# Kernel tuning notes

Hardware: AMD Instinct MI355X
Metric: run time of the kernel (lower is better)

## Reference

```python
import jax, jax.numpy as jnp
import numpy as np

H = 16      # num_heads
D = 64      # head_dim
BQ = 64     # block_size_q
BKV = 64    # block_size_kv


def setup_inputs() -> dict:
    key = jax.random.key(0)
    ks = jax.random.split(key, 5)
    B, S, dim = 2, 2048, 1024
    x = jax.random.normal(ks[0], (B, S, dim), dtype=jnp.float32)
    Wq = jax.random.normal(ks[1], (dim, H * D), dtype=jnp.float32) * 0.02
    Wk = jax.random.normal(ks[2], (dim, H * D), dtype=jnp.float32) * 0.02
    Wv = jax.random.normal(ks[3], (dim, H * D), dtype=jnp.float32) * 0.02
    Wo = jax.random.normal(ks[4], (H * D, dim), dtype=jnp.float32) * 0.02
    return {"x": x, "Wq": Wq, "Wk": Wk, "Wv": Wv, "Wo": Wo}


def _flash_tiled(q, k, v, scale):
    # q,k,v: (B, H, S, D). Non-causal tiled attention with online softmax,
    # faithfully replicating the source's per-iteration division by l_new.
    B, nh, S, d = q.shape
    nq, nkv = S // BQ, S // BKV
    qb = q.reshape(B, nh, nq, BQ, d)                       # all q blocks at once (outer loop vectorized)
    kb = k.reshape(B, nh, nkv, BKV, d).transpose(2, 0, 1, 3, 4)  # (nkv, B, H, BKV, D)
    vb = v.reshape(B, nh, nkv, BKV, d).transpose(2, 0, 1, 3, 4)

    o0 = jnp.zeros((B, nh, nq, BQ, d), q.dtype)
    m0 = jnp.full((B, nh, nq, BQ), -jnp.inf, q.dtype)
    l0 = jnp.zeros((B, nh, nq, BQ), q.dtype)

    def step(carry, kv):
        o, m, l = carry
        kj, vj = kv
        s = jnp.einsum('bhnqd,bhkd->bhnqk', qb, kj) * scale   # (B,H,nq,BQ,BKV)
        m_new = jnp.maximum(m, s.max(axis=-1))
        p = jnp.exp(s - m_new[..., None])
        alpha = jnp.exp(m - m_new)
        l_new = alpha * l + p.sum(axis=-1)
        # NOTE: division by l_new every iteration, as in the source module.
        o_new = (alpha[..., None] * o + jnp.einsum('bhnqk,bhkd->bhnqd', p, vj)) / l_new[..., None]
        return (o_new, m_new, l_new), None

    (o, _, _), _ = jax.lax.scan(step, (o0, m0, l0), (kb, vb))
    return o.reshape(B, nh, S, d)


def reference(x, Wq, Wk, Wv, Wo):
    B, S, dim = x.shape
    scale = D ** -0.5
    q = (x @ Wq).reshape(B, S, H, D).transpose(0, 2, 1, 3)
    k = (x @ Wk).reshape(B, S, H, D).transpose(0, 2, 1, 3)
    v = (x @ Wv).reshape(B, S, H, D).transpose(0, 2, 1, 3)
    o = _flash_tiled(q, k, v, scale)                       # (B,H,S,D)
    out = o.transpose(0, 2, 1, 3).reshape(B, S, H * D)
    return out @ Wo
```

## Files before the change

### kernel.cpp

```cpp
#include <hip/hip_runtime.h>
#include <hip/hip_bf16.h>
#include <math.h>

#define BB   2
#define SS   2048
#define DIM  1024
#define NH   16
#define HD   64
#define MTOT (BB * SS)

typedef unsigned short ushortT;
typedef __attribute__((ext_vector_type(8))) short short8v;
typedef __attribute__((ext_vector_type(4))) float float4v;
typedef __attribute__((ext_vector_type(16))) float float16v;

union FragU { short8v v; unsigned short us[8]; unsigned int u[4]; };

__device__ inline unsigned short f2bf(float x) {
    unsigned u = __builtin_bit_cast(unsigned, x);
    u += 0x7fffu + ((u >> 16) & 1u);
    return (unsigned short)(u >> 16);
}
__device__ inline float bf2f(unsigned short h) {
    unsigned u = ((unsigned)h) << 16;
    return __builtin_bit_cast(float, u);
}
__device__ inline void split_tr(float x, unsigned short& hi, unsigned short& lo) {
    unsigned u = __builtin_bit_cast(unsigned, x);
    hi = (unsigned short)(u >> 16);
    float hf = __builtin_bit_cast(float, u & 0xffff0000u);
    lo = (unsigned short)(__builtin_bit_cast(unsigned, x - hf) >> 16);
}
__device__ inline void split4(const float4& x, short4& hi, short4& lo) {
    unsigned short h0 = f2bf(x.x), h1 = f2bf(x.y), h2 = f2bf(x.z), h3 = f2bf(x.w);
    hi = make_short4((short)h0, (short)h1, (short)h2, (short)h3);
    lo = make_short4((short)f2bf(x.x - bf2f(h0)), (short)f2bf(x.y - bf2f(h1)),
                     (short)f2bf(x.z - bf2f(h2)), (short)f2bf(x.w - bf2f(h3)));
}
__device__ inline void gld_lds16(const void* g, void* l) {
    __builtin_amdgcn_global_load_lds(
        (const __attribute__((address_space(1))) void*)g,
        (__attribute__((address_space(3))) void*)l, 16, 0, 0);
}
__device__ inline unsigned cvt_pk_bf16(float a, float b) {
    unsigned r;
    asm("v_cvt_pk_bf16_f32 %0, %1, %2" : "=v"(r) : "v"(a), "v"(b));
    return r;
}
__device__ inline void permlane32_swap(unsigned &a, unsigned &b) {
    asm("v_permlane32_swap_b32 %0, %1" : "+v"(a), "+v"(b));
}

__global__ __launch_bounds__(256) void convert_split_kernel(
    const float* __restrict__ in, ushortT* __restrict__ hi, ushortT* __restrict__ lo, int n4)
{
    int t = blockIdx.x * 256 + threadIdx.x;
    if (t < n4) {
        float4 x = ((const float4*)in)[t];
        short4 h, l; split4(x, h, l);
        ((short4*)hi)[t] = h;
        ((short4*)lo)[t] = l;
    }
}

__global__ __launch_bounds__(256) void transpose_split_kernel(
    const float* __restrict__ W0, const float* __restrict__ W1,
    const float* __restrict__ W2, const float* __restrict__ W3,
    ushortT* __restrict__ WtH, ushortT* __restrict__ WtL)
{
    const int z = blockIdx.z;
    const float* __restrict__ W = (z == 0) ? W0 : (z == 1) ? W1 : (z == 2) ? W2 : W3;
    ushortT* H = WtH + (size_t)z * 1024 * 1024;
    ushortT* L = WtL + (size_t)z * 1024 * 1024;

    __shared__ float T[64][65];
    const int k0 = blockIdx.y * 64, n0 = blockIdx.x * 64;
    const int tid = threadIdx.x;
    const int c4 = (tid & 15) * 4;

#pragma unroll
    for (int i = 0; i < 4; i++) {
        int r = (tid >> 4) + 16 * i;
        *(float4*)&T[r][c4] = *(const float4*)(W + (size_t)(k0 + r) * 1024 + n0 + c4);
    }
    __syncthreads();
#pragma unroll
    for (int i = 0; i < 4; i++) {
        int n = (tid >> 4) + 16 * i;
        float4 vv = make_float4(T[c4 + 0][n], T[c4 + 1][n], T[c4 + 2][n], T[c4 + 3][n]);
        short4 h, l; split4(vv, h, l);
        *(short4*)&H[(size_t)(n0 + n) * 1024 + k0 + c4] = h;
        *(short4*)&L[(size_t)(n0 + n) * 1024 + k0 + c4] = l;
    }
}

__global__ __launch_bounds__(256) void kv_convert_kernel(
    const float* __restrict__ kw,
    ushortT* __restrict__ KhG, ushortT* __restrict__ KlG)
{
    const int jb = blockIdx.x, bh = blockIdx.y;
    const int b = bh >> 4, h = bh & 15;

    __shared__ float T[64][68];
    const int tid = threadIdx.x;
    const size_t ibase = (size_t)b * SS * DIM + (size_t)h * HD + (size_t)(jb * 64) * DIM;
    const int c4 = (tid & 15) * 4;
#pragma unroll
    for (int i = 0; i < 4; i++) {
        int r = (tid >> 4) + 16 * i;
        *(float4*)&T[r][c4] = *(const float4*)(kw + ibase + (size_t)r * DIM + c4);
    }
    __syncthreads();

    ushortT* oh = KhG + (size_t)(bh * 32 + jb) * 4096;
    ushortT* ol = KlG + (size_t)(bh * 32 + jb) * 4096;

#pragma unroll
    for (int i = 0; i < 2; i++) {
        const int s = tid + i * 256;
        const int f = s >> 6;
        const int lane = s & 63;
        const int ds = f >> 1, kvt = f & 1;
        const int kv = kvt * 32 + (lane & 31);
        const int d0 = ds * 16 + (lane >> 5) * 8;
        ushortT hv[8], lv[8];
#pragma unroll
        for (int j = 0; j < 8; j++) split_tr(T[kv][d0 + j], hv[j], lv[j]);
        *(short4*)&oh[s * 8]     = *(short4*)&hv[0];
        *(short4*)&oh[s * 8 + 4] = *(short4*)&hv[4];
        *(short4*)&ol[s * 8]     = *(short4*)&lv[0];
        *(short4*)&ol[s * 8 + 4] = *(short4*)&lv[4];
    }
}

__global__ __launch_bounds__(256, 2) void gemm_bt_split_kernel(
    const ushortT* __restrict__ Ah, const ushortT* __restrict__ Al,
    const ushortT* __restrict__ BtH, const ushortT* __restrict__ BtL,
    float* __restrict__ Y0, float* __restrict__ Y1,
    ushortT* __restrict__ VhG, ushortT* __restrict__ VlG)
{
    const int z = blockIdx.z;
    const ushortT* __restrict__ Bh = BtH + (size_t)z * 1024 * 1024;
    const ushortT* __restrict__ Bl = BtL + (size_t)z * 1024 * 1024;

    const int K = 1024, N = 1024;
    const int m0 = blockIdx.y * 128;
    const int n0 = blockIdx.x * 128;

    __shared__ __align__(16) ushortT AhS[128 * 32];
    __shared__ __align__(16) ushortT AlS[128 * 32];
    __shared__ __align__(16) ushortT BhS[128 * 32];
    __shared__ __align__(16) ushortT BlS[128 * 32];

    const int tid  = threadIdx.x;
    const int wave = tid >> 6, lane = tid & 63;
    const int quad = lane >> 4, l15 = lane & 15;
    const int wm = wave >> 1, wn = wave & 1;

    const int s0 = tid, s1 = tid + 256;
    const int ar0 = s0 >> 2, ak0 = (s0 & 3) * 8;
    const int ar1 = s1 >> 2, ak1 = (s1 & 3) * 8;

    float4v acc[4][4];
#pragma unroll
    for (int i = 0; i < 4; i++)
#pragma unroll
        for (int j = 0; j < 4; j++) acc[i][j] = (float4v){0.f, 0.f, 0.f, 0.f};

    for (int k0 = 0; k0 < K; k0 += 32) {
        __syncthreads();
        gld_lds16(Ah + (size_t)(m0 + ar0) * K + k0 + ak0, &AhS[s0 * 8]);
        gld_lds16(Ah + (size_t)(m0 + ar1) * K + k0 + ak1, &AhS[s1 * 8]);
        gld_lds16(Al + (size_t)(m0 + ar0) * K + k0 + ak0, &AlS[s0 * 8]);
        gld_lds16(Al + (size_t)(m0 + ar1) * K + k0 + ak1, &AlS[s1 * 8]);
        gld_lds16(Bh + (size_t)(n0 + ar0) * K + k0 + ak0, &BhS[s0 * 8]);
        gld_lds16(Bh + (size_t)(n0 + ar1) * K + k0 + ak1, &BhS[s1 * 8]);
        gld_lds16(Bl + (size_t)(n0 + ar0) * K + k0 + ak0, &BlS[s0 * 8]);
        gld_lds16(Bl + (size_t)(n0 + ar1) * K + k0 + ak1, &BlS[s1 * 8]);
        __syncthreads();

        FragU ah[4], al[4], bh[4], bl[4];
#pragma unroll
        for (int t = 0; t < 4; t++) {
            ah[t].v = *(const short8v*)&AhS[(wm * 64 + t * 16 + l15) * 32 + quad * 8];
            al[t].v = *(const short8v*)&AlS[(wm * 64 + t * 16 + l15) * 32 + quad * 8];
            bh[t].v = *(const short8v*)&BhS[(wn * 64 + t * 16 + l15) * 32 + quad * 8];
            bl[t].v = *(const short8v*)&BlS[(wn * 64 + t * 16 + l15) * 32 + quad * 8];
        }
#pragma unroll
        for (int mt = 0; mt < 4; mt++)
#pragma unroll
            for (int nt = 0; nt < 4; nt++) {
                acc[mt][nt] = __builtin_amdgcn_mfma_f32_16x16x32_bf16(ah[mt].v, bh[nt].v, acc[mt][nt], 0, 0, 0);
                acc[mt][nt] = __builtin_amdgcn_mfma_f32_16x16x32_bf16(ah[mt].v, bl[nt].v, acc[mt][nt], 0, 0, 0);
                acc[mt][nt] = __builtin_amdgcn_mfma_f32_16x16x32_bf16(al[mt].v, bh[nt].v, acc[mt][nt], 0, 0, 0);
            }
    }

    if (z == 2) {
        const int b  = m0 >> 11;
        const int jb = ((m0 & 2047) >> 6) + wm;
        const int h  = (n0 >> 6) + wn;
        const size_t tb = (size_t)((b * 16 + h) * 32 + jb) * 4096;
        ushortT* vh = VhG + tb;
        ushortT* vl = VlG + tb;
#pragma unroll
        for (int mt = 0; mt < 4; mt++)
#pragma unroll
            for (int nt = 0; nt < 4; nt++) {
                const int off = ((((nt >> 1) * 4 + mt) * 64 +
                                  (quad >> 1) * 32 + (nt & 1) * 16 + l15) * 8) +
                                (quad & 1) * 4;
                float4 vv = make_float4(acc[mt][nt][0], acc[mt][nt][1],
                                        acc[mt][nt][2], acc[mt][nt][3]);
                unsigned short h0, l0, h1, l1, h2, l2, h3, l3;
                split_tr(vv.x, h0, l0); split_tr(vv.y, h1, l1);
                split_tr(vv.z, h2, l2); split_tr(vv.w, h3, l3);
                *(short4*)&vh[off] = make_short4((short)h0, (short)h1, (short)h2, (short)h3);
                *(short4*)&vl[off] = make_short4((short)l0, (short)l1, (short)l2, (short)l3);
            }
    } else {
        float* __restrict__ Y = (z == 0) ? Y0 : Y1;
#pragma unroll
        for (int mt = 0; mt < 4; mt++)
#pragma unroll
            for (int r = 0; r < 4; r++) {
                const int row = m0 + wm * 64 + mt * 16 + quad * 4 + r;
                float* yp = Y + (size_t)row * N + n0 + wn * 64 + l15;
#pragma unroll
                for (int nt = 0; nt < 4; nt++)
                    yp[nt * 16] = acc[mt][nt][r];
            }
    }
}

__global__ __launch_bounds__(256, 3) void attn_mfma_kernel(
    const float* __restrict__ q,
    const ushortT* __restrict__ KhG, const ushortT* __restrict__ KlG,
    const ushortT* __restrict__ VhG, const ushortT* __restrict__ VlG,
    ushortT* __restrict__ Oh, ushortT* __restrict__ Ol)
{
    __shared__ __align__(16) ushortT SMEM[16384];
    ushortT* KhS = SMEM;
    ushortT* KlS = SMEM + 4096;
    ushortT* VhS = SMEM + 8192;
    ushortT* VlS = SMEM + 12288;

    const int tid  = threadIdx.x;
    const int wave = tid >> 6, lane = tid & 63;
    const int l31 = lane & 31, hi5 = lane >> 5;
    const int bh = blockIdx.y, b = bh >> 4, h = bh & 15;
    const size_t base = (size_t)b * SS * DIM + (size_t)h * HD;
    const int qs0 = blockIdx.x * 128 + wave * 32;
    const int lane8 = lane * 8;

    const float qscale = 0.125f * 1.4426950408889634f;
    FragU Qh[4], Ql[4];
    {
        const int qrow = qs0 + l31;
#pragma unroll
        for (int ds = 0; ds < 4; ds++) {
            const float* p0 = q + base + (size_t)qrow * DIM + ds * 16 + hi5 * 8;
            float4 a = *(const float4*)(p0);
            float4 c = *(const float4*)(p0 + 4);
            float e[8] = {a.x, a.y, a.z, a.w, c.x, c.y, c.z, c.w};
#pragma unroll
            for (int j = 0; j < 8; j++) {
                float x = e[j] * qscale;
                unsigned short hs = f2bf(x);
                Qh[ds].us[j] = hs;
                Ql[ds].us[j] = f2bf(x - bf2f(hs));
            }
        }
    }

    float16v Oacc[2];
#pragma unroll
    for (int dt = 0; dt < 2; dt++)
        Oacc[dt] = (float16v){0.f,0.f,0.f,0.f,0.f,0.f,0.f,0.f,
                              0.f,0.f,0.f,0.f,0.f,0.f,0.f,0.f};

    float m_run = -INFINITY;
    float l_run = 0.f;

    const int sl0 = wave * 128 + lane, sl1 = sl0 + 64;

    for (int jb = 0; jb < 32; jb++) {
        __syncthreads();
        {
            const size_t tb = (size_t)(bh * 32 + jb) * 4096;
            gld_lds16(KhG + tb + sl0 * 8, &KhS[sl0 * 8]);
            gld_lds16(KhG + tb + sl1 * 8, &KhS[sl1 * 8]);
            gld_lds16(KlG + tb + sl0 * 8, &KlS[sl0 * 8]);
            gld_lds16(KlG + tb + sl1 * 8, &KlS[sl1 * 8]);
            gld_lds16(VhG + tb + sl0 * 8, &VhS[sl0 * 8]);
            gld_lds16(VhG + tb + sl1 * 8, &VhS[sl1 * 8]);
            gld_lds16(VlG + tb + sl0 * 8, &VlS[sl0 * 8]);
            gld_lds16(VlG + tb + sl1 * 8, &VlS[sl1 * 8]);
        }
        __syncthreads();

        float16v st[2];
#pragma unroll
        for (int t = 0; t < 2; t++)
            st[t] = (float16v){0.f,0.f,0.f,0.f,0.f,0.f,0.f,0.f,
                               0.f,0.f,0.f,0.f,0.f,0.f,0.f,0.f};

#pragma unroll
        for (int ds = 0; ds < 4; ds++) {
            FragU kh0, kl0, kh1, kl1;
            kh0.v = *(const short8v*)&KhS[(ds * 2 + 0) * 512 + lane8];
            kl0.v = *(const short8v*)&KlS[(ds * 2 + 0) * 512 + lane8];
            kh1.v = *(const short8v*)&KhS[(ds * 2 + 1) * 512 + lane8];
            kl1.v = *(const short8v*)&KlS[(ds * 2 + 1) * 512 + lane8];
            st[0] = __builtin_amdgcn_mfma_f32_32x32x16_bf16(kh0.v, Qh[ds].v, st[0], 0, 0, 0);
            st[0] = __builtin_amdgcn_mfma_f32_32x32x16_bf16(kh0.v, Ql[ds].v, st[0], 0, 0, 0);
            st[0] = __builtin_amdgcn_mfma_f32_32x32x16_bf16(kl0.v, Qh[ds].v, st[0], 0, 0, 0);
            st[1] = __builtin_amdgcn_mfma_f32_32x32x16_bf16(kh1.v, Qh[ds].v, st[1], 0, 0, 0);
            st[1] = __builtin_amdgcn_mfma_f32_32x32x16_bf16(kh1.v, Ql[ds].v, st[1], 0, 0, 0);
            st[1] = __builtin_amdgcn_mfma_f32_32x32x16_bf16(kl1.v, Qh[ds].v, st[1], 0, 0, 0);
        }

        float oscale, inv;
        {
            float g[8];
#pragma unroll
            for (int t = 0; t < 2; t++)
#pragma unroll
                for (int i = 0; i < 4; i++)
                    g[t * 4 + i] = fmaxf(fmaxf(st[t][4 * i], st[t][4 * i + 1]),
                                         fmaxf(st[t][4 * i + 2], st[t][4 * i + 3]));
            float vmax = fmaxf(fmaxf(fmaxf(g[0], g[1]), fmaxf(g[2], g[3])),
                               fmaxf(fmaxf(g[4], g[5]), fmaxf(g[6], g[7])));
            vmax = fmaxf(vmax, __shfl_xor(vmax, 32, 64));
            const float mn = fmaxf(m_run, vmax);
            const float al = __builtin_amdgcn_exp2f(m_run - mn);

            float ssum = 0.f;
#pragma unroll
            for (int t = 0; t < 2; t++)
#pragma unroll
                for (int r = 0; r < 16; r++) {
                    const float p = __builtin_amdgcn_exp2f(st[t][r] - mn);
                    st[t][r] = p;
                    ssum += p;
                }
            ssum += __shfl_xor(ssum, 32, 64);
            const float ln = al * l_run + ssum;
            inv = __builtin_amdgcn_rcpf(ln);
            oscale = al * inv;
#pragma unroll
            for (int t = 0; t < 2; t++)
#pragma unroll
                for (int r = 0; r < 16; r++)
                    st[t][r] *= inv;
            m_run = mn;
            l_run = ln;
        }

#pragma unroll
        for (int dt = 0; dt < 2; dt++)
#pragma unroll
            for (int r = 0; r < 16; r++)
                Oacc[dt][r] *= oscale;

#pragma unroll
        for (int kvs = 0; kvs < 4; kvs++) {
            const int kvt = kvs >> 1;
            const int R = (kvs & 1) * 8;
            float p0 = st[kvt][R + 0], p1 = st[kvt][R + 1];
            float p2 = st[kvt][R + 2], p3 = st[kvt][R + 3];
            float p4 = st[kvt][R + 4], p5 = st[kvt][R + 5];
            float p6 = st[kvt][R + 6], p7 = st[kvt][R + 7];
            unsigned X0 = cvt_pk_bf16(p0, p1), X1 = cvt_pk_bf16(p2, p3);
            unsigned Y0 = cvt_pk_bf16(p4, p5), Y1 = cvt_pk_bf16(p6, p7);
            float e0 = p0 - __builtin_bit_cast(float, X0 << 16);
            float e1 = p1 - __builtin_bit_cast(float, X0 & 0xffff0000u);
            float e2 = p2 - __builtin_bit_cast(float, X1 << 16);
            float e3 = p3 - __builtin_bit_cast(float, X1 & 0xffff0000u);
            float e4 = p4 - __builtin_bit_cast(float, Y0 << 16);
            float e5 = p5 - __builtin_bit_cast(float, Y0 & 0xffff0000u);
            float e6 = p6 - __builtin_bit_cast(float, Y1 << 16);
            float e7 = p7 - __builtin_bit_cast(float, Y1 & 0xffff0000u);
            unsigned Z0 = cvt_pk_bf16(e0, e1), Z1 = cvt_pk_bf16(e2, e3);
            unsigned W0 = cvt_pk_bf16(e4, e5), W1 = cvt_pk_bf16(e6, e7);
            permlane32_swap(X0, Y0);
            permlane32_swap(X1, Y1);
            permlane32_swap(Z0, W0);
            permlane32_swap(Z1, W1);
            FragU Phf, Plf;
            Phf.u[0] = X0; Phf.u[1] = X1; Phf.u[2] = Y0; Phf.u[3] = Y1;
            Plf.u[0] = Z0; Plf.u[1] = Z1; Plf.u[2] = W0; Plf.u[3] = W1;

#pragma unroll
            for (int dt = 0; dt < 2; dt++) {
                FragU vh, vl;
                vh.v = *(const short8v*)&VhS[(dt * 4 + kvs) * 512 + lane8];
                vl.v = *(const short8v*)&VlS[(dt * 4 + kvs) * 512 + lane8];
                Oacc[dt] = __builtin_amdgcn_mfma_f32_32x32x16_bf16(vh.v, Phf.v, Oacc[dt], 0, 0, 0);
                Oacc[dt] = __builtin_amdgcn_mfma_f32_32x32x16_bf16(vl.v, Phf.v, Oacc[dt], 0, 0, 0);
                Oacc[dt] = __builtin_amdgcn_mfma_f32_32x32x16_bf16(vh.v, Plf.v, Oacc[dt], 0, 0, 0);
            }
        }
    }

    __syncthreads();
    float* EP = ((float*)SMEM) + wave * 1056;
    const int qq = lane >> 1, dh = (lane & 1) * 16;
#pragma unroll
    for (int dt = 0; dt < 2; dt++) {
#pragma unroll
        for (int g = 0; g < 4; g++) {
            float4 wv = make_float4(Oacc[dt][4 * g + 0], Oacc[dt][4 * g + 1],
                                    Oacc[dt][4 * g + 2], Oacc[dt][4 * g + 3]);
            *(float4*)&EP[l31 * 33 + g * 8 + hi5 * 4] = wv;
        }
        float vals[16];
#pragma unroll
        for (int k4 = 0; k4 < 4; k4++)
            *(float4*)&vals[k4 * 4] = *(const float4*)&EP[qq * 33 + dh + k4 * 4];

        unsigned ho[8], lo8[8];
#pragma unroll
        for (int kk = 0; kk < 8; kk++) {
            unsigned short h0, l0, h1, l1;
            split_tr(vals[2 * kk], h0, l0);
            split_tr(vals[2 * kk + 1], h1, l1);
            ho[kk]  = (unsigned)h0 | ((unsigned)h1 << 16);
            lo8[kk] = (unsigned)l0 | ((unsigned)l1 << 16);
        }
        const int qrow = qs0 + qq;
        const size_t off = (size_t)(b * SS + qrow) * DIM + h * HD + dt * 32 + dh;
        *(uint4*)&Oh[off]     = make_uint4(ho[0], ho[1], ho[2], ho[3]);
        *(uint4*)&Oh[off + 8] = make_uint4(ho[4], ho[5], ho[6], ho[7]);
        *(uint4*)&Ol[off]     = make_uint4(lo8[0], lo8[1], lo8[2], lo8[3]);
        *(uint4*)&Ol[off + 8] = make_uint4(lo8[4], lo8[5], lo8[6], lo8[7]);
    }
}

extern "C" void kernel_launch(void* const* d_in, const int* in_sizes, int n_in,
                              void* d_out, int out_size, void* d_ws, size_t ws_size,
                              hipStream_t stream)
{
    const float* x  = (const float*)d_in[0];
    const float* Wq = (const float*)d_in[1];
    const float* Wk = (const float*)d_in[2];
    const float* Wv = (const float*)d_in[3];
    const float* Wo = (const float*)d_in[4];
    float* out = (float*)d_out;

    char* w = (char*)d_ws;
    float*   qw  = (float*)(w);
    float*   kw  = (float*)(w + ((size_t)16 << 20));
    ushortT* VhG = (ushortT*)(w + ((size_t)32 << 20));
    ushortT* VlG = (ushortT*)(w + ((size_t)40 << 20));
    ushortT* XhS = (ushortT*)(w + ((size_t)48 << 20));
    ushortT* XlS = (ushortT*)(w + ((size_t)56 << 20));
    ushortT* WtH = (ushortT*)(w + ((size_t)64 << 20));
    ushortT* WtL = (ushortT*)(w + ((size_t)72 << 20));
    ushortT* KhG = (ushortT*)(w + ((size_t)80 << 20));
    ushortT* KlG = (ushortT*)(w + ((size_t)88 << 20));
    ushortT* OhS = (ushortT*)kw;
    ushortT* OlS = (ushortT*)(w + ((size_t)24 << 20));

    dim3 blk(256);
    const int n4 = MTOT * DIM / 4;

    convert_split_kernel<<<dim3(n4 / 256), blk, 0, stream>>>(x, XhS, XlS, n4);
    transpose_split_kernel<<<dim3(16, 16, 4), blk, 0, stream>>>(Wq, Wk, Wv, Wo, WtH, WtL);

    gemm_bt_split_kernel<<<dim3(8, 32, 3), blk, 0, stream>>>(
        XhS, XlS, WtH, WtL, qw, kw, VhG, VlG);

    kv_convert_kernel<<<dim3(32, 32), blk, 0, stream>>>(kw, KhG, KlG);

    attn_mfma_kernel<<<dim3(16, 32), blk, 0, stream>>>(qw, KhG, KlG, VhG, VlG, OhS, OlS);

    gemm_bt_split_kernel<<<dim3(8, 32, 1), blk, 0, stream>>>(
        OhS, OlS, WtH + (size_t)3 * 1024 * 1024, WtL + (size_t)3 * 1024 * 1024,
        out, nullptr, nullptr, nullptr);
}
```

Baseline: 324.1 us.

## Double-buffer K/V tiles in LDS to overlap loads with attention compute

The attention kernel now keeps two LDS buffers for the hi/lo K and V tiles. It issues the direct global-to-LDS loads for the next KV block before computing on the current one, and synchronises once per iteration instead of twice. The goal is to hide global load latency behind the MFMA work. LDS use doubles to 64 KB per block and the launch bound drops from 3 to 2 blocks per CU, so occupancy falls. Correctness also depends on the async LDS loads having completed when the single barrier is reached.

```diff
diff --git a/kernel.cpp b/kernel.cpp
--- a/kernel.cpp
+++ b/kernel.cpp
@@ -234,17 +234,13 @@
     }
 }
 
-__global__ __launch_bounds__(256, 3) void attn_mfma_kernel(
+__global__ __launch_bounds__(256, 2) void attn_mfma_kernel(
     const float* __restrict__ q,
     const ushortT* __restrict__ KhG, const ushortT* __restrict__ KlG,
     const ushortT* __restrict__ VhG, const ushortT* __restrict__ VlG,
     ushortT* __restrict__ Oh, ushortT* __restrict__ Ol)
 {
-    __shared__ __align__(16) ushortT SMEM[16384];
-    ushortT* KhS = SMEM;
-    ushortT* KlS = SMEM + 4096;
-    ushortT* VhS = SMEM + 8192;
-    ushortT* VlS = SMEM + 12288;
+    __shared__ __align__(16) ushortT SMEM[32768];
 
     const int tid  = threadIdx.x;
     const int wave = tid >> 6, lane = tid & 63;
@@ -253,6 +249,7 @@
     const size_t base = (size_t)b * SS * DIM + (size_t)h * HD;
     const int qs0 = blockIdx.x * 128 + wave * 32;
     const int lane8 = lane * 8;
+    const int sl0 = wave * 128 + lane, sl1 = sl0 + 64;
 
     const float qscale = 0.125f * 1.4426950408889634f;
     FragU Qh[4], Ql[4];
@@ -283,22 +280,30 @@
     float m_run = -INFINITY;
     float l_run = 0.f;
 
-    const int sl0 = wave * 128 + lane, sl1 = sl0 + 64;
+    auto stage = [&](int bbuf, int jb) {
+        const size_t tb = (size_t)(bh * 32 + jb) * 4096;
+        ushortT* S = SMEM + bbuf * 16384;
+        gld_lds16(KhG + tb + sl0 * 8, &S[sl0 * 8]);
+        gld_lds16(KhG + tb + sl1 * 8, &S[sl1 * 8]);
+        gld_lds16(KlG + tb + sl0 * 8, &S[4096 + sl0 * 8]);
+        gld_lds16(KlG + tb + sl1 * 8, &S[4096 + sl1 * 8]);
+        gld_lds16(VhG + tb + sl0 * 8, &S[8192 + sl0 * 8]);
+        gld_lds16(VhG + tb + sl1 * 8, &S[8192 + sl1 * 8]);
+        gld_lds16(VlG + tb + sl0 * 8, &S[12288 + sl0 * 8]);
+        gld_lds16(VlG + tb + sl1 * 8, &S[12288 + sl1 * 8]);
+    };
+
+    stage(0, 0);
+    __syncthreads();
+    int bb = 0;
 
     for (int jb = 0; jb < 32; jb++) {
-        __syncthreads();
-        {
-            const size_t tb = (size_t)(bh * 32 + jb) * 4096;
-            gld_lds16(KhG + tb + sl0 * 8, &KhS[sl0 * 8]);
-            gld_lds16(KhG + tb + sl1 * 8, &KhS[sl1 * 8]);
-            gld_lds16(KlG + tb + sl0 * 8, &KlS[sl0 * 8]);
-            gld_lds16(KlG + tb + sl1 * 8, &KlS[sl1 * 8]);
-            gld_lds16(VhG + tb + sl0 * 8, &VhS[sl0 * 8]);
-            gld_lds16(VhG + tb + sl1 * 8, &VhS[sl1 * 8]);
-            gld_lds16(VlG + tb + sl0 * 8, &VlS[sl0 * 8]);
-            gld_lds16(VlG + tb + sl1 * 8, &VlS[sl1 * 8]);
-        }
-        __syncthreads();
+        if (jb < 31) stage(bb ^ 1, jb + 1);
+
+        const ushortT* KhS = SMEM + bb * 16384;
+        const ushortT* KlS = KhS + 4096;
+        const ushortT* VhS = KhS + 8192;
+        const ushortT* VlS = KhS + 12288;
 
         float16v st[2];
 #pragma unroll
@@ -402,9 +407,11 @@
                 Oacc[dt] = __builtin_amdgcn_mfma_f32_32x32x16_bf16(vh.v, Plf.v, Oacc[dt], 0, 0, 0);
             }
         }
-    }
-
-    __syncthreads();
+
+        __syncthreads();
+        bb ^= 1;
+    }
+
     float* EP = ((float*)SMEM) + wave * 1056;
     const int qq = lane >> 1, dh = (lane & 1) * 16;
 #pragma unroll
```

Measured after the change: 326.3 us. About the same (+0.7%).
